# Optimization experiments

Measured on AMD Instinct MI355X. Metric: run time of the kernel, lower is better.

Reference implementation:

```python
import jax, jax.numpy as jnp
import numpy as np

HIDDEN = 512
INPUT = 128
SEQ = 512
BATCH = 128
ALPHA = 0.5          # dt / tau = 1 / 2
NOISE_STD = 0.05


def setup_inputs() -> dict:
    key = jax.random.key(0)
    k_x, k_wi, k_wh, k_n = jax.random.split(key, 4)
    inp = jax.random.normal(k_x, (SEQ, BATCH, INPUT), dtype=jnp.float32)
    # input layer: uniform dist (as in LinearLayer default 'uniform'), no bias
    lim = 1.0 / np.sqrt(INPUT)
    W_in = jax.random.uniform(k_wi, (HIDDEN, INPUT), minval=-lim, maxval=lim, dtype=jnp.float32)
    # hidden layer: normal dist, scaled ~ 1/sqrt(N) for unit spectral radius
    W_hid = jax.random.normal(k_wh, (HIDDEN, HIDDEN), dtype=jnp.float32) / np.sqrt(HIDDEN)
    # per-step noise, shared across batch, pre-scaled by std
    noise = jax.random.normal(k_n, (SEQ, HIDDEN), dtype=jnp.float32) * NOISE_STD
    return {"input": inp, "W_in": W_in, "W_hid": W_hid, "noise": noise}


def reference(input, W_in, W_hid, noise):
    # pre-compute the input projection for all steps: (S, B, H)
    proj_in = jnp.einsum('sbi,hi->sbh', input, W_in)

    def step(h, xs):
        x_t, n_t = xs                      # (B,H), (H,)
        hidden_out = jnp.einsum('bh,gh->bg', jax.nn.relu(h), W_hid)
        h_new = (1.0 - ALPHA) * h + ALPHA * (hidden_out + x_t + n_t)
        return h_new, h_new

    h0 = jnp.zeros((input.shape[1], HIDDEN), dtype=input.dtype)
    hidden, output = jax.lax.scan(step, h0, (proj_in, noise))
    return output, hidden
```

## Files before the change

### kernel.cpp

```cpp
#include <hip/hip_runtime.h>
#include <hip/hip_bf16.h>


#define SEQ   512
#define NB    128
#define NI    128
#define NH    512
#define WBG   8
#define WGG   16
#define BT    16
#define GT    32

typedef __attribute__((ext_vector_type(8))) short  short8;
typedef __attribute__((ext_vector_type(4))) float  float4v;
typedef __attribute__((ext_vector_type(4))) int    int4v;
typedef __attribute__((ext_vector_type(2))) int    int2v;

static __device__ __forceinline__ unsigned short f2bf(float f) {
    __hip_bfloat16 h = __float2bfloat16(f);
    unsigned short u;
    __builtin_memcpy(&u, &h, 2);
    return u;
}

static __device__ __forceinline__ short8 pack8(float4v a, float4v b) {
    short8 r;
    r[0] = (short)f2bf(a[0]); r[1] = (short)f2bf(a[1]);
    r[2] = (short)f2bf(a[2]); r[3] = (short)f2bf(a[3]);
    r[4] = (short)f2bf(b[0]); r[5] = (short)f2bf(b[1]);
    r[6] = (short)f2bf(b[2]); r[7] = (short)f2bf(b[3]);
    return r;
}

#define LOADR(idx, off) \
    asm volatile("global_load_dwordx4 %0, %1, off offset:" #off " sc0 sc1" \
                 : "=v"(rv[idx]) : "v"(rbase));

__global__ __launch_bounds__(64, 1) void rnn_step_kernel(
    const float* __restrict__ xin,
    const float* __restrict__ w_in,
    const float* __restrict__ w_hid,
    const float* __restrict__ noise,
    float*       __restrict__ out,
    unsigned int*              cnt,
    unsigned short*            xbuf)
{
    const int lane = threadIdx.x;
    const int r16  = lane & 15;
    const int kg   = lane >> 4;
    const int ib   = blockIdx.x & 7;
    const int jg   = blockIdx.x >> 3;
    const int b0   = ib * BT;
    const int g0   = jg * GT;

    short8 wf[2][16];
#pragma unroll
    for (int t = 0; t < 2; ++t)
#pragma unroll
        for (int c = 0; c < 16; ++c) {
            const float* p = w_hid + (size_t)(g0 + t * 16 + r16) * NH + c * 32 + kg * 8;
            wf[t][c] = pack8(*(const float4v*)p, *(const float4v*)(p + 4));
        }
    short8 wfin[2][4];
#pragma unroll
    for (int t = 0; t < 2; ++t)
#pragma unroll
        for (int c = 0; c < 4; ++c) {
            const float* p = w_in + (size_t)(g0 + t * 16 + r16) * NI + c * 32 + kg * 8;
            wfin[t][c] = pack8(*(const float4v*)p, *(const float4v*)(p + 4));
        }

    float4v h0 = {0.f, 0.f, 0.f, 0.f};
    float4v h1 = {0.f, 0.f, 0.f, 0.f};

    const float* inp  = xin + (size_t)(b0 + r16) * NI + kg * 8;
    const float* nzp  = noise + g0 + kg * 4;
    float*       outp = out + (size_t)(b0 + r16) * NH + g0 + kg * 4;

    const unsigned long long xbase  = (unsigned long long)(uintptr_t)xbuf;
    const unsigned long long xw_off = ((unsigned long long)(b0 + r16) * NH + g0 + kg * 4) * 2ull;
    const unsigned long long xr_off = ((unsigned long long)(b0 + r16) * NH + kg * 8) * 2ull;
    const unsigned long long bufstride = (unsigned long long)NB * NH * 2ull;

#pragma unroll 1
    for (int s = 0; s < SEQ; ++s) {
        const float* ip = inp + (size_t)s * NB * NI;
        short8 bin[4];
#pragma unroll
        for (int c = 0; c < 4; ++c) {
            float4v a = *(const float4v*)(ip + c * 32);
            float4v b = *(const float4v*)(ip + c * 32 + 4);
            bin[c] = pack8(a, b);
        }
        const float* np_ = nzp + (size_t)s * NH;
        float4v nz0 = *(const float4v*)np_;
        float4v nz1 = *(const float4v*)(np_ + 16);

        float4v acc0 = {0.f, 0.f, 0.f, 0.f};
        float4v acc1 = {0.f, 0.f, 0.f, 0.f};
#pragma unroll
        for (int c = 0; c < 4; ++c) {
            acc0 = __builtin_amdgcn_mfma_f32_16x16x32_bf16(wfin[0][c], bin[c], acc0, 0, 0, 0);
            acc1 = __builtin_amdgcn_mfma_f32_16x16x32_bf16(wfin[1][c], bin[c], acc1, 0, 0, 0);
        }

        if (s > 0) {
            const unsigned int* cp = cnt + (size_t)(s - 1) * WBG + ib;
            unsigned int v;
            unsigned int guard = 0;
            do {
                v = __hip_atomic_load(cp, __ATOMIC_RELAXED, __HIP_MEMORY_SCOPE_AGENT);
            } while (v < (unsigned)WGG && ++guard < (1u << 20));
            __builtin_amdgcn_sched_barrier(0);

            unsigned long long rbase = xbase + (unsigned long long)((s - 1) & 1) * bufstride + xr_off;
            int4v rv[16];
            LOADR(0, 0)   LOADR(1, 64)   LOADR(2, 128)  LOADR(3, 192)
            LOADR(4, 256) LOADR(5, 320)  LOADR(6, 384)  LOADR(7, 448)
            LOADR(8, 512) LOADR(9, 576)  LOADR(10, 640) LOADR(11, 704)
            LOADR(12, 768) LOADR(13, 832) LOADR(14, 896) LOADR(15, 960)
            asm volatile("s_waitcnt vmcnt(0)"
                         : "+v"(rv[0]), "+v"(rv[1]), "+v"(rv[2]), "+v"(rv[3]),
                           "+v"(rv[4]), "+v"(rv[5]), "+v"(rv[6]), "+v"(rv[7]),
                           "+v"(rv[8]), "+v"(rv[9]), "+v"(rv[10]), "+v"(rv[11]),
                           "+v"(rv[12]), "+v"(rv[13]), "+v"(rv[14]), "+v"(rv[15])
                         :
                         : "memory");
            __builtin_amdgcn_sched_barrier(0);

#pragma unroll
            for (int c = 0; c < 16; ++c) {
                short8 rb = __builtin_bit_cast(short8, rv[c]);
                acc0 = __builtin_amdgcn_mfma_f32_16x16x32_bf16(wf[0][c], rb, acc0, 0, 0, 0);
                acc1 = __builtin_amdgcn_mfma_f32_16x16x32_bf16(wf[1][c], rb, acc1, 0, 0, 0);
            }
        }

        float4v hn0, hn1;
#pragma unroll
        for (int r = 0; r < 4; ++r) {
            hn0[r] = 0.5f * h0[r] + 0.5f * (acc0[r] + nz0[r]);
            hn1[r] = 0.5f * h1[r] + 0.5f * (acc1[r] + nz1[r]);
        }
        h0 = hn0; h1 = hn1;

        unsigned int q0 = (unsigned)f2bf(fmaxf(hn0[0], 0.f)) | ((unsigned)f2bf(fmaxf(hn0[1], 0.f)) << 16);
        unsigned int q1 = (unsigned)f2bf(fmaxf(hn0[2], 0.f)) | ((unsigned)f2bf(fmaxf(hn0[3], 0.f)) << 16);
        unsigned int q2 = (unsigned)f2bf(fmaxf(hn1[0], 0.f)) | ((unsigned)f2bf(fmaxf(hn1[1], 0.f)) << 16);
        unsigned int q3 = (unsigned)f2bf(fmaxf(hn1[2], 0.f)) | ((unsigned)f2bf(fmaxf(hn1[3], 0.f)) << 16);
        int2v e0; e0[0] = (int)q0; e0[1] = (int)q1;
        int2v e1; e1[0] = (int)q2; e1[1] = (int)q3;
        unsigned long long wb = xbase + (unsigned long long)(s & 1) * bufstride + xw_off;
        asm volatile("global_store_dwordx2 %0, %1, off sc0 sc1" :: "v"(wb), "v"(e0) : "memory");
        asm volatile("global_store_dwordx2 %0, %1, off offset:32 sc0 sc1" :: "v"(wb), "v"(e1) : "memory");
        asm volatile("s_waitcnt vmcnt(0)" ::: "memory");
        if (lane == 0) {
            __hip_atomic_fetch_add(cnt + (size_t)s * WBG + ib, 1u,
                                   __ATOMIC_RELAXED, __HIP_MEMORY_SCOPE_AGENT);
        }

        float* op = outp + (size_t)s * NB * NH;
        *(float4v*)op        = hn0;
        *(float4v*)(op + 16) = hn1;
        if (s == SEQ - 1) {
            float* tp = out + (size_t)SEQ * NB * NH + (size_t)(b0 + r16) * NH + g0 + kg * 4;
            *(float4v*)tp        = hn0;
            *(float4v*)(tp + 16) = hn1;
        }
    }
}

extern "C" void kernel_launch(void* const* d_in, const int* in_sizes, int n_in,
                              void* d_out, int out_size, void* d_ws, size_t ws_size,
                              hipStream_t stream) {
    (void)in_sizes; (void)n_in; (void)out_size; (void)ws_size;
    const float* xin   = (const float*)d_in[0];
    const float* w_in  = (const float*)d_in[1];
    const float* w_hid = (const float*)d_in[2];
    const float* noise = (const float*)d_in[3];
    float* out = (float*)d_out;

    unsigned int*   cnt  = (unsigned int*)d_ws;
    unsigned short* xbuf = (unsigned short*)((char*)d_ws + SEQ * WBG * sizeof(unsigned int));

    hipMemsetAsync(d_ws, 0, SEQ * WBG * sizeof(unsigned int), stream);
    hipLaunchKernelGGL(rnn_step_kernel, dim3(WBG * WGG), dim3(64), 0, stream,
                       xin, w_in, w_hid, noise, out, cnt, xbuf);
}
```

Measured before the change: 1.669 ms.

## Replace atomic counter barrier with tag bits embedded in exchanged bf16 data

Drops the per-step atomic counter handshake between workgroups. Each stored bf16 hidden value now carries a parity tag in its sign bit, which is free because the ReLU output is non-negative. Readers poll the data buffer itself until every value shows the expected tag, then clear the tag bits before the MFMAs. This removes one store-wait, atomic, poll, then load round trip per step, at the cost of repeated 1KB reloads while spinning and a memset pattern that must never match a valid tag. The recurrent MFMA chain is also split into four independent accumulators to shorten the dependency chain.

After: 1.471 ms. 1.13x faster.

```diff
diff --git a/kernel.cpp b/kernel.cpp
--- a/kernel.cpp
+++ b/kernel.cpp
@@ -42,7 +42,6 @@
     const float* __restrict__ w_hid,
     const float* __restrict__ noise,
     float*       __restrict__ out,
-    unsigned int*              cnt,
     unsigned short*            xbuf)
 {
     const int lane = threadIdx.x;
@@ -105,34 +104,63 @@
         }
 
         if (s > 0) {
-            const unsigned int* cp = cnt + (size_t)(s - 1) * WBG + ib;
-            unsigned int v;
-            unsigned int guard = 0;
-            do {
-                v = __hip_atomic_load(cp, __ATOMIC_RELAXED, __HIP_MEMORY_SCOPE_AGENT);
-            } while (v < (unsigned)WGG && ++guard < (1u << 20));
-            __builtin_amdgcn_sched_barrier(0);
-
+            const unsigned expTag = ((unsigned)(s - 1) >> 1) & 1u;
             unsigned long long rbase = xbase + (unsigned long long)((s - 1) & 1) * bufstride + xr_off;
             int4v rv[16];
-            LOADR(0, 0)   LOADR(1, 64)   LOADR(2, 128)  LOADR(3, 192)
-            LOADR(4, 256) LOADR(5, 320)  LOADR(6, 384)  LOADR(7, 448)
-            LOADR(8, 512) LOADR(9, 576)  LOADR(10, 640) LOADR(11, 704)
-            LOADR(12, 768) LOADR(13, 832) LOADR(14, 896) LOADR(15, 960)
-            asm volatile("s_waitcnt vmcnt(0)"
-                         : "+v"(rv[0]), "+v"(rv[1]), "+v"(rv[2]), "+v"(rv[3]),
-                           "+v"(rv[4]), "+v"(rv[5]), "+v"(rv[6]), "+v"(rv[7]),
-                           "+v"(rv[8]), "+v"(rv[9]), "+v"(rv[10]), "+v"(rv[11]),
-                           "+v"(rv[12]), "+v"(rv[13]), "+v"(rv[14]), "+v"(rv[15])
-                         :
-                         : "memory");
+            unsigned guard = 0;
+            for (;;) {
+                LOADR(0, 0)    LOADR(1, 64)   LOADR(2, 128)  LOADR(3, 192)
+                LOADR(4, 256)  LOADR(5, 320)  LOADR(6, 384)  LOADR(7, 448)
+                LOADR(8, 512)  LOADR(9, 576)  LOADR(10, 640) LOADR(11, 704)
+                LOADR(12, 768) LOADR(13, 832) LOADR(14, 896) LOADR(15, 960)
+                asm volatile("s_waitcnt vmcnt(0)"
+                             : "+v"(rv[0]), "+v"(rv[1]), "+v"(rv[2]), "+v"(rv[3]),
+                               "+v"(rv[4]), "+v"(rv[5]), "+v"(rv[6]), "+v"(rv[7]),
+                               "+v"(rv[8]), "+v"(rv[9]), "+v"(rv[10]), "+v"(rv[11]),
+                               "+v"(rv[12]), "+v"(rv[13]), "+v"(rv[14]), "+v"(rv[15])
+                             :
+                             : "memory");
+                bool ok;
+                if (expTag) {
+                    unsigned a = 0xFFFFFFFFu;
+#pragma unroll
+                    for (int c = 0; c < 16; ++c)
+                        a &= (unsigned)(rv[c][0] & rv[c][1] & rv[c][2] & rv[c][3]);
+                    ok = (a & 0x80008000u) == 0x80008000u;
+                } else {
+                    unsigned o = 0u;
+#pragma unroll
+                    for (int c = 0; c < 16; ++c)
+                        o |= (unsigned)(rv[c][0] | rv[c][1] | rv[c][2] | rv[c][3]);
+                    ok = (o & 0x80008000u) == 0u;
+                }
+                if (__all(ok) || ++guard >= (1u << 16)) break;
+            }
             __builtin_amdgcn_sched_barrier(0);
 
-#pragma unroll
-            for (int c = 0; c < 16; ++c) {
-                short8 rb = __builtin_bit_cast(short8, rv[c]);
-                acc0 = __builtin_amdgcn_mfma_f32_16x16x32_bf16(wf[0][c], rb, acc0, 0, 0, 0);
-                acc1 = __builtin_amdgcn_mfma_f32_16x16x32_bf16(wf[1][c], rb, acc1, 0, 0, 0);
+            if (expTag) {
+#pragma unroll
+                for (int c = 0; c < 16; ++c) {
+                    rv[c][0] &= 0x7FFF7FFF; rv[c][1] &= 0x7FFF7FFF;
+                    rv[c][2] &= 0x7FFF7FFF; rv[c][3] &= 0x7FFF7FFF;
+                }
+            }
+
+            float4v p0a = {0.f,0.f,0.f,0.f}, p0b = {0.f,0.f,0.f,0.f};
+            float4v p1a = {0.f,0.f,0.f,0.f}, p1b = {0.f,0.f,0.f,0.f};
+#pragma unroll
+            for (int c = 0; c < 8; ++c) {
+                short8 rb0 = __builtin_bit_cast(short8, rv[c]);
+                short8 rb1 = __builtin_bit_cast(short8, rv[c + 8]);
+                p0a = __builtin_amdgcn_mfma_f32_16x16x32_bf16(wf[0][c],     rb0, p0a, 0, 0, 0);
+                p0b = __builtin_amdgcn_mfma_f32_16x16x32_bf16(wf[0][c + 8], rb1, p0b, 0, 0, 0);
+                p1a = __builtin_amdgcn_mfma_f32_16x16x32_bf16(wf[1][c],     rb0, p1a, 0, 0, 0);
+                p1b = __builtin_amdgcn_mfma_f32_16x16x32_bf16(wf[1][c + 8], rb1, p1b, 0, 0, 0);
+            }
+#pragma unroll
+            for (int r = 0; r < 4; ++r) {
+                acc0[r] += p0a[r] + p0b[r];
+                acc1[r] += p1a[r] + p1b[r];
             }
         }
 
@@ -144,20 +172,17 @@
         }
         h0 = hn0; h1 = hn1;
 
-        unsigned int q0 = (unsigned)f2bf(fmaxf(hn0[0], 0.f)) | ((unsigned)f2bf(fmaxf(hn0[1], 0.f)) << 16);
-        unsigned int q1 = (unsigned)f2bf(fmaxf(hn0[2], 0.f)) | ((unsigned)f2bf(fmaxf(hn0[3], 0.f)) << 16);
-        unsigned int q2 = (unsigned)f2bf(fmaxf(hn1[0], 0.f)) | ((unsigned)f2bf(fmaxf(hn1[1], 0.f)) << 16);
-        unsigned int q3 = (unsigned)f2bf(fmaxf(hn1[2], 0.f)) | ((unsigned)f2bf(fmaxf(hn1[3], 0.f)) << 16);
+        const unsigned tmask = ((s >> 1) & 1) ? 0x80008000u : 0u;
+        unsigned q0 = ((unsigned)f2bf(fmaxf(hn0[0], 0.f)) | ((unsigned)f2bf(fmaxf(hn0[1], 0.f)) << 16)) | tmask;
+        unsigned q1 = ((unsigned)f2bf(fmaxf(hn0[2], 0.f)) | ((unsigned)f2bf(fmaxf(hn0[3], 0.f)) << 16)) | tmask;
+        unsigned q2 = ((unsigned)f2bf(fmaxf(hn1[0], 0.f)) | ((unsigned)f2bf(fmaxf(hn1[1], 0.f)) << 16)) | tmask;
+        unsigned q3 = ((unsigned)f2bf(fmaxf(hn1[2], 0.f)) | ((unsigned)f2bf(fmaxf(hn1[3], 0.f)) << 16)) | tmask;
         int2v e0; e0[0] = (int)q0; e0[1] = (int)q1;
         int2v e1; e1[0] = (int)q2; e1[1] = (int)q3;
         unsigned long long wb = xbase + (unsigned long long)(s & 1) * bufstride + xw_off;
+        asm volatile("s_waitcnt vmcnt(0)" ::: "memory");
         asm volatile("global_store_dwordx2 %0, %1, off sc0 sc1" :: "v"(wb), "v"(e0) : "memory");
         asm volatile("global_store_dwordx2 %0, %1, off offset:32 sc0 sc1" :: "v"(wb), "v"(e1) : "memory");
-        asm volatile("s_waitcnt vmcnt(0)" ::: "memory");
-        if (lane == 0) {
-            __hip_atomic_fetch_add(cnt + (size_t)s * WBG + ib, 1u,
-                                   __ATOMIC_RELAXED, __HIP_MEMORY_SCOPE_AGENT);
-        }
 
         float* op = outp + (size_t)s * NB * NH;
         *(float4v*)op        = hn0;
@@ -180,10 +205,9 @@
     const float* noise = (const float*)d_in[3];
     float* out = (float*)d_out;
 
-    unsigned int*   cnt  = (unsigned int*)d_ws;
-    unsigned short* xbuf = (unsigned short*)((char*)d_ws + SEQ * WBG * sizeof(unsigned int));
-
-    hipMemsetAsync(d_ws, 0, SEQ * WBG * sizeof(unsigned int), stream);
+    unsigned short* xbuf = (unsigned short*)d_ws;
+
+    hipMemsetAsync(d_ws, 0xAA, 2 * NB * NH * sizeof(unsigned short), stream);
     hipLaunchKernelGGL(rnn_step_kernel, dim3(WBG * WGG), dim3(64), 0, stream,
-                       xin, w_in, w_hid, noise, out, cnt, xbuf);
-}
+                       xin, w_in, w_hid, noise, out, xbuf);
+}
```
